# Kernel optimization log

Measured on AMD Instinct MI355X. Metric: run time of the kernel, lower is better.

## Reference

```python
import jax, jax.numpy as jnp
import numpy as np

B, S, D, H, DFF = 2, 4096, 256, 8, 1024
DK = D // H


def setup_inputs() -> dict:
    key = jax.random.key(0)
    ks = jax.random.split(key, 12)
    sc = 0.02
    inp = {
        "x": jax.random.normal(ks[0], (B, S, D), jnp.float32),
        "mask": jnp.ones((B, 1, 1, S), jnp.int32),
        "Wq": jax.random.normal(ks[1], (D, D), jnp.float32) * sc,
        "bq": jnp.zeros((D,), jnp.float32),
        "Wk": jax.random.normal(ks[2], (D, D), jnp.float32) * sc,
        "bk": jnp.zeros((D,), jnp.float32),
        "Wv": jax.random.normal(ks[3], (D, D), jnp.float32) * sc,
        "bv": jnp.zeros((D,), jnp.float32),
        "Wo": jax.random.normal(ks[4], (D, D), jnp.float32) * sc,
        "bo": jnp.zeros((D,), jnp.float32),
        "W1": jax.random.normal(ks[5], (D, DFF), jnp.float32) * sc,
        "b1": jnp.zeros((DFF,), jnp.float32),
        "W2": jax.random.normal(ks[6], (DFF, D), jnp.float32) * sc,
        "b2": jnp.zeros((D,), jnp.float32),
        "g1": jnp.ones((D,), jnp.float32),
        "be1": jnp.zeros((D,), jnp.float32),
        "g2": jnp.ones((D,), jnp.float32),
        "be2": jnp.zeros((D,), jnp.float32),
        "a1": jnp.float32(1e-8),
        "a2": jnp.float32(1e-8),
    }
    return inp


def _layernorm(x, g, b, eps=1e-5):
    mu = jnp.mean(x, axis=-1, keepdims=True)
    var = jnp.var(x, axis=-1, keepdims=True)
    return (x - mu) * jax.lax.rsqrt(var + eps) * g + b


def _block(x, mask, Wq, bq, Wk, bk, Wv, bv, Wo, bo, W1, b1, W2, b2, g1, be1, g2, be2, a1, a2):
    # multi-head attention (dropout = identity in eval)
    def proj(W, b):
        return (x @ W + b).reshape(B, S, H, DK).transpose(0, 2, 1, 3)  # [B,H,S,DK]
    q, k, v = proj(Wq, bq), proj(Wk, bk), proj(Wv, bv)
    scores = jnp.einsum("bhsd,bhtd->bhst", q, k) / jnp.sqrt(jnp.float32(DK))
    scores = jnp.where(mask == 0, jnp.float32(-1e9), scores)
    p_attn = jax.nn.softmax(scores, axis=-1)
    ctx = jnp.einsum("bhst,bhtd->bhsd", p_attn, v)
    ctx = ctx.transpose(0, 2, 1, 3).reshape(B, S, D)
    attn_out = ctx @ Wo + bo
    x1 = _layernorm(x + a1 * attn_out, g1, be1)
    # FFN
    h = jax.nn.gelu(x1 @ W1 + b1, approximate=False)
    ffn_out = h @ W2 + b2
    return _layernorm(x1 + a2 * ffn_out, g2, be2)


def reference(x, mask, Wq, bq, Wk, bk, Wv, bv, Wo, bo, W1, b1, W2, b2, g1, be1, g2, be2, a1, a2):
    return _block(x, mask, Wq, bq, Wk, bk, Wv, bv, Wo, bo, W1, b1, W2, b2, g1, be1, g2, be2, a1, a2)
```

## Files before the change

### kernel.cpp

```cpp
#include <hip/hip_runtime.h>
#include <hip/hip_bf16.h>
#include <math.h>

#define B_ 2
#define S_ 4096
#define D_ 256
#define H_ 8
#define DFF_ 1024
#define DK_ 32

typedef __attribute__((ext_vector_type(8))) short short8;
typedef __attribute__((ext_vector_type(4))) float f32x4;
typedef __attribute__((ext_vector_type(16))) float f32x16;
typedef __attribute__((ext_vector_type(4))) int int4v;

__device__ __forceinline__ unsigned short f2bf(float f) {
  unsigned int u = __builtin_bit_cast(unsigned int, f);
  u += 0x7FFFu + ((u >> 16) & 1u);
  return (unsigned short)(u >> 16);
}

__device__ __forceinline__ float bf2f(unsigned short s) {
  unsigned int u = ((unsigned int)s) << 16;
  return __builtin_bit_cast(float, u);
}

__device__ __forceinline__ short8 u32x4_to_s8(unsigned int a, unsigned int b,
                                              unsigned int c, unsigned int d) {
  int4v v = {(int)a, (int)b, (int)c, (int)d};
  return __builtin_bit_cast(short8, v);
}

__device__ __forceinline__ float gelu_fast(float v) {
  float e = __builtin_amdgcn_exp2f(v * fmaf(0.10294609f, v * v, 2.3022077f));
  float th = 1.0f - 2.0f * __builtin_amdgcn_rcpf(e + 1.0f);
  return 0.5f * v * (1.0f + th);
}

__global__ __launch_bounds__(256) void k_prepw(
    const float* __restrict__ Wq, const float* __restrict__ Wk,
    const float* __restrict__ Wv, const float* __restrict__ Wo,
    const float* __restrict__ W1, const float* __restrict__ W2,
    const float* __restrict__ bq, const float* __restrict__ bk,
    const float* __restrict__ bv, const float* __restrict__ x,
    unsigned short* __restrict__ WqkvT, unsigned short* __restrict__ WoT,
    unsigned short* __restrict__ W1pk, unsigned short* __restrict__ W2pk,
    float* __restrict__ bqkv, unsigned short* __restrict__ xb) {
  const float k2 = 0.25500525551f;
  int bx = blockIdx.x, t = threadIdx.x;

  if (bx < 192) {
    __shared__ float tile[64][65];
    const float* src;
    int Nsz, ti, tj;
    float scale = 1.0f;
    if (bx < 48) {
      int which = bx >> 4, s = bx & 15;
      src = (which == 0) ? Wq : (which == 1) ? Wk : Wv;
      Nsz = 256; ti = s >> 2; tj = s & 3;
      if (which == 0) scale = k2;
    } else if (bx < 64) {
      int s = bx - 48;
      src = Wo; Nsz = 256; ti = s >> 2; tj = s & 3;
    } else if (bx < 128) {
      int s = bx - 64;
      src = W1; Nsz = 1024; ti = s >> 4; tj = s & 15;
    } else {
      int s = bx - 128;
      src = W2; Nsz = 256; ti = s >> 2; tj = s & 3;
    }
    int row0 = ti * 64, col0 = tj * 64;
    int c = t & 63, rg = t >> 6;
#pragma unroll
    for (int i = 0; i < 16; i++) {
      int rr = rg * 16 + i;
      tile[rr][c] = src[(size_t)(row0 + rr) * Nsz + col0 + c] * scale;
    }
    __syncthreads();

    if (bx < 64) {
      unsigned short* dst;
      if (bx < 48) dst = WqkvT + (bx >> 4) * 65536;
      else dst = WoT;
      int k = t & 63;
#pragma unroll
      for (int i = 0; i < 16; i++) {
        int nn = rg * 16 + i;
        dst[(size_t)(col0 + nn) * 256 + row0 + k] = f2bf(tile[k][nn]);
      }
    } else {
      unsigned short* pk = (bx < 128) ? W1pk : W2pk;
      int kst_tot = (bx < 128) ? 8 : 32;
      int lane2 = t & 63, sub2 = t >> 6;
#pragma unroll
      for (int i = 0; i < 2; i++) {
        int subc = sub2 * 2 + i;
        int ntl = subc >> 1, kst = subc & 1;
        short8 o;
#pragma unroll
        for (int e = 0; e < 8; e++)
          o[e] = (short)f2bf(tile[kst * 32 + (lane2 >> 4) * 8 + e][ntl * 16 + (lane2 & 15)]);
        int ntg = tj * 4 + ntl;
        int ksg = ti * 2 + kst;
        *(short8*)(pk + ((size_t)(ntg * kst_tot + ksg) * 64 + lane2) * 8) = o;
      }
    }
  } else if (bx == 192) {
#pragma unroll
    for (int j = 0; j < 3; j++) {
      int i = j * 256 + t;
      if (i < 768)
        bqkv[i] = (i < 256) ? bq[i] * k2 : (i < 512) ? bk[i - 256] : bv[i - 512];
    }
  } else {
    int i = (bx - 193) * 2048 + t * 8;
    f32x4 f0 = *(const f32x4*)(x + i);
    f32x4 f1 = *(const f32x4*)(x + i + 4);
    short8 o;
#pragma unroll
    for (int e = 0; e < 4; e++) { o[e] = (short)f2bf(f0[e]); o[e + 4] = (short)f2bf(f1[e]); }
    *(short8*)(xb + i) = o;
  }
}

__global__ __launch_bounds__(256) void k_gemmqkv(const unsigned short* __restrict__ A,
                                                 const unsigned short* __restrict__ Bt,
                                                 const float* __restrict__ bias,
                                                 unsigned short* __restrict__ qb,
                                                 unsigned short* __restrict__ kpk,
                                                 unsigned short* __restrict__ vpk) {
  const int K = 256;
  __shared__ unsigned short Al[128][40];
  __shared__ unsigned short Bl[128][40];
  const int tid = threadIdx.x;
  const int wid = tid >> 6, lane = tid & 63;
  const int lhi = lane >> 4, llo = lane & 15;
  const int wr = wid >> 1, wc = wid & 1;
  const int rowbase = wr * 64, colbase = wc * 64;
  const int bm = blockIdx.x, bn = blockIdx.y;

  f32x4 zero = {0.f, 0.f, 0.f, 0.f};
  f32x4 acc[4][4];
#pragma unroll
  for (int m = 0; m < 4; m++)
#pragma unroll
    for (int n = 0; n < 4; n++) acc[m][n] = zero;

  const int r0 = tid >> 2, c8 = (tid & 3) * 8;
  const unsigned short* A16a = A + (size_t)(bm * 128 + r0) * K + c8;
  const unsigned short* A16b = A + (size_t)(bm * 128 + r0 + 64) * K + c8;
  const unsigned short* Brow0 = Bt + (size_t)(bn * 128 + r0) * K + c8;
  const unsigned short* Brow1 = Bt + (size_t)(bn * 128 + r0 + 64) * K + c8;

  for (int kb = 0; kb < K; kb += 32) {
    __syncthreads();
    *(short8*)&Al[r0][c8] = *(const short8*)(A16a + kb);
    *(short8*)&Al[r0 + 64][c8] = *(const short8*)(A16b + kb);
    *(short8*)&Bl[r0][c8] = *(const short8*)(Brow0 + kb);
    *(short8*)&Bl[r0 + 64][c8] = *(const short8*)(Brow1 + kb);
    __syncthreads();
    short8 af[4], bf[4];
#pragma unroll
    for (int m = 0; m < 4; m++) af[m] = *(const short8*)&Al[rowbase + m * 16 + llo][lhi * 8];
#pragma unroll
    for (int n = 0; n < 4; n++) bf[n] = *(const short8*)&Bl[colbase + n * 16 + llo][lhi * 8];
#pragma unroll
    for (int m = 0; m < 4; m++)
#pragma unroll
      for (int n = 0; n < 4; n++)
        acc[m][n] = __builtin_amdgcn_mfma_f32_16x16x32_bf16(af[m], bf[n], acc[m][n], 0, 0, 0);
  }

#pragma unroll
  for (int m = 0; m < 4; m++)
#pragma unroll
    for (int n = 0; n < 4; n++)
#pragma unroll
      for (int r = 0; r < 4; r++) {
        int row = bm * 128 + rowbase + m * 16 + lhi * 4 + r;
        int gcol = bn * 128 + colbase + n * 16 + llo;
        int which = gcol >> 8;
        int col0 = gcol & 255;
        float v = acc[m][n][r] + bias[gcol];
        unsigned short bv = f2bf(v);
        int t = row & (S_ - 1), b = row >> 12;
        int h = col0 >> 5;
        if (which == 0) {
          qb[(size_t)row * 256 + col0] = bv;
        } else if (which == 1) {
          int c5 = col0 & 31, jj = (c5 >> 4) & 1, hik = (c5 >> 3) & 1, e = c5 & 7;
          int tile = t >> 6, i = (t >> 5) & 1, l31k = t & 31;
          size_t addr = (((size_t)(b * 8 + h) * 64 + tile) * 4 + i * 2 + jj) * 512 +
                        (hik * 32 + l31k) * 8 + e;
          kpk[addr] = bv;
        } else {
          int d = col0 & 31;
          int x5 = t >> 6, j = (t >> 3) & 7, kk = t & 7;
          size_t addr = (((size_t)(b * 8 + h) * 64 + x5) * 4 + (j >> 1)) * 512 +
                        ((j & 1) * 32 + d) * 8 + kk;
          vpk[addr] = bv;
        }
      }
}

__global__ __launch_bounds__(512) void k_ffn(const unsigned short* __restrict__ x1b,
                                             const unsigned short* __restrict__ W1pk,
                                             const float* __restrict__ b1,
                                             const unsigned short* __restrict__ W2pk,
                                             const float* __restrict__ b2,
                                             const float* __restrict__ alpha,
                                             const float* __restrict__ g,
                                             const float* __restrict__ be,
                                             float* __restrict__ out) {
  __shared__ unsigned short Ax[32][268];
  __shared__ unsigned short Hl[32][268];
  __shared__ float psum[32][8], psq[32][8];
  const int tid = threadIdx.x;
  const int w = tid >> 6, lane = tid & 63;
  const int lhi = lane >> 4, llo = lane & 15;
  const int row0 = blockIdx.x * 32;

  {
    int r = tid >> 4, c0 = (tid & 15) * 16;
    const unsigned short* src = x1b + (size_t)(row0 + r) * 256 + c0;
    *(short8*)&Ax[r][c0] = *(const short8*)(src);
    *(short8*)&Ax[r][c0 + 8] = *(const short8*)(src + 8);
  }
  __syncthreads();

  f32x4 zero4 = {0.f, 0.f, 0.f, 0.f};
  f32x4 acc2[2][2];
#pragma unroll
  for (int m = 0; m < 2; m++)
#pragma unroll
    for (int n = 0; n < 2; n++) acc2[m][n] = zero4;

  for (int c = 0; c < 4; ++c) {
    f32x4 acc1[2][2];
#pragma unroll
    for (int m = 0; m < 2; m++)
#pragma unroll
      for (int n = 0; n < 2; n++) acc1[m][n] = zero4;
    const unsigned short* w1base = W1pk + (size_t)(c * 16 + w * 2) * 4096 + lane * 8;
#pragma unroll
    for (int kb = 0; kb < 8; ++kb) {
      short8 af0 = *(const short8*)&Ax[llo][kb * 32 + lhi * 8];
      short8 af1 = *(const short8*)&Ax[16 + llo][kb * 32 + lhi * 8];
      short8 bf0 = *(const short8*)(w1base + kb * 512);
      short8 bf1 = *(const short8*)(w1base + 4096 + kb * 512);
      acc1[0][0] = __builtin_amdgcn_mfma_f32_16x16x32_bf16(af0, bf0, acc1[0][0], 0, 0, 0);
      acc1[0][1] = __builtin_amdgcn_mfma_f32_16x16x32_bf16(af0, bf1, acc1[0][1], 0, 0, 0);
      acc1[1][0] = __builtin_amdgcn_mfma_f32_16x16x32_bf16(af1, bf0, acc1[1][0], 0, 0, 0);
      acc1[1][1] = __builtin_amdgcn_mfma_f32_16x16x32_bf16(af1, bf1, acc1[1][1], 0, 0, 0);
    }
    __syncthreads();
#pragma unroll
    for (int m = 0; m < 2; m++)
#pragma unroll
      for (int n = 0; n < 2; n++)
#pragma unroll
        for (int r = 0; r < 4; r++) {
          int col = w * 32 + n * 16 + llo;
          float v = acc1[m][n][r] + b1[c * 256 + col];
          Hl[m * 16 + lhi * 4 + r][col] = f2bf(gelu_fast(v));
        }
    __syncthreads();
    const unsigned short* w2base = W2pk + (size_t)(w * 2) * 16384 + (size_t)(c * 8) * 512 + lane * 8;
#pragma unroll
    for (int kk = 0; kk < 8; ++kk) {
      short8 a0 = *(const short8*)&Hl[llo][kk * 32 + lhi * 8];
      short8 a1 = *(const short8*)&Hl[16 + llo][kk * 32 + lhi * 8];
      short8 bf0 = *(const short8*)(w2base + kk * 512);
      short8 bf1 = *(const short8*)(w2base + 16384 + kk * 512);
      acc2[0][0] = __builtin_amdgcn_mfma_f32_16x16x32_bf16(a0, bf0, acc2[0][0], 0, 0, 0);
      acc2[0][1] = __builtin_amdgcn_mfma_f32_16x16x32_bf16(a0, bf1, acc2[0][1], 0, 0, 0);
      acc2[1][0] = __builtin_amdgcn_mfma_f32_16x16x32_bf16(a1, bf0, acc2[1][0], 0, 0, 0);
      acc2[1][1] = __builtin_amdgcn_mfma_f32_16x16x32_bf16(a1, bf1, acc2[1][1], 0, 0, 0);
    }
  }

  const float a = alpha[0];
#pragma unroll
  for (int m = 0; m < 2; m++)
#pragma unroll
    for (int r = 0; r < 4; r++) {
      int lrow = m * 16 + lhi * 4 + r;
      float s = 0.f, q = 0.f;
#pragma unroll
      for (int n = 0; n < 2; n++) {
        int col = w * 32 + n * 16 + llo;
        float v = acc2[m][n][r] + b2[col];
        float xv = bf2f(Ax[lrow][col]);
        float rr = fmaf(a, v, xv);
        acc2[m][n][r] = rr;
        s += rr;
        q = fmaf(rr, rr, q);
      }
#pragma unroll
      for (int off = 1; off < 16; off <<= 1) {
        s += __shfl_xor(s, off);
        q += __shfl_xor(q, off);
      }
      if (llo == 0) { psum[lrow][w] = s; psq[lrow][w] = q; }
    }
  __syncthreads();
#pragma unroll
  for (int m = 0; m < 2; m++)
#pragma unroll
    for (int r = 0; r < 4; r++) {
      int lrow = m * 16 + lhi * 4 + r;
      size_t grow = (size_t)(row0 + lrow);
      float S = 0.f, Q = 0.f;
#pragma unroll
      for (int j = 0; j < 8; j++) { S += psum[lrow][j]; Q += psq[lrow][j]; }
      float mu = S * (1.0f / 256.0f);
      float var = Q * (1.0f / 256.0f) - mu * mu;
      float rs = rsqrtf(var + 1e-5f);
#pragma unroll
      for (int n = 0; n < 2; n++) {
        int col = w * 32 + n * 16 + llo;
        out[grow * 256 + col] = (acc2[m][n][r] - mu) * rs * g[col] + be[col];
      }
    }
}

template <int BASE16, int OUT32>
__global__ __launch_bounds__(512) void k_gemmln(const unsigned short* __restrict__ A,
                                                const unsigned short* __restrict__ Bt,
                                                const float* __restrict__ bias,
                                                const void* __restrict__ base,
                                                const float* __restrict__ alpha,
                                                const float* __restrict__ g,
                                                const float* __restrict__ be,
                                                void* __restrict__ y, int K) {
  __shared__ unsigned short Al[2][32][40];
  __shared__ unsigned short Bl[2][256][40];
  __shared__ float psum[32][4], psq[32][4];
  float* partial = (float*)&Bl[0][0][0];

  const int tid = threadIdx.x;
  const int w = tid >> 6, lane = tid & 63;
  const int kh = w >> 2, wc = w & 3;
  const int lhi = lane >> 4, llo = lane & 15;
  const int row0 = blockIdx.x * 32;
  const int Kh = K >> 1;

  f32x4 zero = {0.f, 0.f, 0.f, 0.f};
  f32x4 acc[2][4];
#pragma unroll
  for (int m = 0; m < 2; m++)
#pragma unroll
    for (int n = 0; n < 4; n++) acc[m][n] = zero;

  for (int kb = 0; kb < Kh; kb += 32) {
    __syncthreads();
    if (tid < 256) {
      int kh2 = tid >> 7, ra = (tid >> 2) & 31, ca = (tid & 3) * 8;
      *(short8*)&Al[kh2][ra][ca] =
          *(const short8*)(A + (size_t)(row0 + ra) * K + kh2 * Kh + kb + ca);
    }
#pragma unroll
    for (int s = 0; s < 4; s++) {
      int c = tid + s * 512;
      int kh2 = c >> 10, rb = (c >> 2) & 255, cb = (c & 3) * 8;
      *(short8*)&Bl[kh2][rb][cb] =
          *(const short8*)(Bt + (size_t)rb * K + kh2 * Kh + kb + cb);
    }
    __syncthreads();
    short8 af[2], bf[4];
#pragma unroll
    for (int m = 0; m < 2; m++) af[m] = *(const short8*)&Al[kh][m * 16 + llo][lhi * 8];
#pragma unroll
    for (int n = 0; n < 4; n++)
      bf[n] = *(const short8*)&Bl[kh][wc * 64 + n * 16 + llo][lhi * 8];
#pragma unroll
    for (int m = 0; m < 2; m++)
#pragma unroll
      for (int n = 0; n < 4; n++)
        acc[m][n] = __builtin_amdgcn_mfma_f32_16x16x32_bf16(af[m], bf[n], acc[m][n], 0, 0, 0);
  }

  __syncthreads();
  if (kh == 1) {
#pragma unroll
    for (int m = 0; m < 2; m++)
#pragma unroll
      for (int n = 0; n < 4; n++)
#pragma unroll
        for (int r = 0; r < 4; r++) {
          int lrow = m * 16 + lhi * 4 + r;
          int col = wc * 64 + n * 16 + llo;
          partial[lrow * 256 + col] = acc[m][n][r];
        }
  }
  __syncthreads();

  const float a = alpha[0];
  const unsigned short* b16 = (const unsigned short*)base;
  const float* b32 = (const float*)base;

  if (kh == 0) {
#pragma unroll
    for (int m = 0; m < 2; m++)
#pragma unroll
      for (int r = 0; r < 4; r++) {
        int lrow = m * 16 + lhi * 4 + r;
        size_t grow = (size_t)(row0 + lrow);
        float s = 0.f, q = 0.f;
#pragma unroll
        for (int n = 0; n < 4; n++) {
          int col = wc * 64 + n * 16 + llo;
          float v = acc[m][n][r] + partial[lrow * 256 + col] + bias[col];
          float xb = BASE16 ? bf2f(b16[grow * 256 + col]) : b32[grow * 256 + col];
          float rr = fmaf(a, v, xb);
          acc[m][n][r] = rr;
          s += rr;
          q = fmaf(rr, rr, q);
        }
#pragma unroll
        for (int off = 1; off < 16; off <<= 1) {
          s += __shfl_xor(s, off);
          q += __shfl_xor(q, off);
        }
        if (llo == 0) { psum[lrow][wc] = s; psq[lrow][wc] = q; }
      }
  }
  __syncthreads();

  if (kh == 0) {
#pragma unroll
    for (int m = 0; m < 2; m++)
#pragma unroll
      for (int r = 0; r < 4; r++) {
        int lrow = m * 16 + lhi * 4 + r;
        size_t grow = (size_t)(row0 + lrow);
        float S = psum[lrow][0] + psum[lrow][1] + psum[lrow][2] + psum[lrow][3];
        float Q = psq[lrow][0] + psq[lrow][1] + psq[lrow][2] + psq[lrow][3];
        float mu = S * (1.0f / 256.0f);
        float var = Q * (1.0f / 256.0f) - mu * mu;
        float rs = rsqrtf(var + 1e-5f);
#pragma unroll
        for (int n = 0; n < 4; n++) {
          int col = wc * 64 + n * 16 + llo;
          float o = (acc[m][n][r] - mu) * rs * g[col] + be[col];
          if (OUT32) ((float*)y)[grow * 256 + col] = o;
          else ((unsigned short*)y)[grow * 256 + col] = f2bf(o);
        }
      }
  }
}

__global__ __launch_bounds__(256, 2) void k_attn(const unsigned short* __restrict__ qbuf,
                                                 const unsigned short* __restrict__ kpk,
                                                 const unsigned short* __restrict__ vpk,
                                                 const int* __restrict__ mask,
                                                 unsigned short* __restrict__ ctx) {
  __shared__ float accS[4][64][32];
  __shared__ float lS[4][64];
  const int tid = threadIdx.x;
  const int lane = tid & 63;
  const int w = tid >> 6;
  const int l31 = lane & 31, hi = lane >> 5;
  const int q0 = blockIdx.x * 64;
  const int h = blockIdx.y, b = blockIdx.z;
  const size_t bS = (size_t)b * S_;

  const unsigned short* QpA = qbuf + (bS + q0 + l31) * 256 + h * DK_ + hi * 8;
  short8 qa0 = *(const short8*)QpA;
  short8 qa1 = *(const short8*)(QpA + 16);
  const unsigned short* QpB = QpA + 32 * 256;
  short8 qb0 = *(const short8*)QpB;
  short8 qb1 = *(const short8*)(QpB + 16);

  const size_t fragbase = ((size_t)(b * H_ + h) * 64 + w * 16) * 2048 + lane * 8;
  const unsigned short* kp = kpk + fragbase;
  const unsigned short* vp = vpk + fragbase;
  const int* mp = mask + bS + w * 1024 + lane;

  f32x16 accA, accB, laccA, laccB;
#pragma unroll
  for (int r = 0; r < 16; r++) { accA[r] = 0.f; accB[r] = 0.f; laccA[r] = 0.f; laccB[r] = 0.f; }
  const f32x16 zz = accA;
  short8 ones;
#pragma unroll
  for (int e = 0; e < 8; e++) ones[e] = (short)0x3F80;

  short8 kA[4], vA[4], kB[4], vB[4];
  unsigned int pk0[8], pk1[8];
  f32x16 s0, s1;
  int tcur = 0;
  int mvC, mvN;

#define LDK(DST) { DST[0] = *(const short8*)(kp); DST[1] = *(const short8*)(kp + 512); \
                   DST[2] = *(const short8*)(kp + 1024); DST[3] = *(const short8*)(kp + 1536); kp += 2048; }
#define LDV(DST) { DST[0] = *(const short8*)(vp); DST[1] = *(const short8*)(vp + 512); \
                   DST[2] = *(const short8*)(vp + 1024); DST[3] = *(const short8*)(vp + 1536); vp += 2048; }
#define QKM(KF, qx0, qx1) {                                                      \
    s0 = __builtin_amdgcn_mfma_f32_32x32x16_bf16(KF[0], qx0, zz, 0, 0, 0);       \
    s1 = __builtin_amdgcn_mfma_f32_32x32x16_bf16(KF[2], qx0, zz, 0, 0, 0);       \
    s0 = __builtin_amdgcn_mfma_f32_32x32x16_bf16(KF[1], qx1, s0, 0, 0, 0);       \
    s1 = __builtin_amdgcn_mfma_f32_32x32x16_bf16(KF[3], qx1, s1, 0, 0, 0);       \
  }
#define EXPM(bal) {                                                              \
    if (__builtin_expect((bal) != ~0ull, 0)) {                                   \
      _Pragma("unroll") for (int r = 0; r < 16; r++) {                           \
        int tt = (r & 3) + 8 * (r >> 2) + 4 * hi;                                \
        if (!(((bal) >> tt) & 1)) s0[r] = -3e38f;                                \
        if (!(((bal) >> (tt + 32)) & 1)) s1[r] = -3e38f;                         \
      }                                                                          \
    }                                                                            \
    _Pragma("unroll") for (int r = 0; r < 16; r++) {                             \
      s0[r] = __builtin_amdgcn_exp2f(s0[r]);                                     \
      s1[r] = __builtin_amdgcn_exp2f(s1[r]);                                     \
    }                                                                            \
    _Pragma("unroll") for (int j = 0; j < 8; j++) {                              \
      asm("v_cvt_pk_bf16_f32 %0, %1, %2" : "=v"(pk0[j]) : "v"(s0[2*j]), "v"(s0[2*j+1])); \
      asm("v_cvt_pk_bf16_f32 %0, %1, %2" : "=v"(pk1[j]) : "v"(s1[2*j]), "v"(s1[2*j+1])); \
    }                                                                            \
  }
#define PVM(VF, accX, laccX) {                                                   \
    __builtin_amdgcn_s_setprio(1);                                               \
    _Pragma("unroll") for (int kk = 0; kk < 4; kk++) {                           \
      unsigned int* pk = (kk < 2) ? pk0 : pk1;                                   \
      int base = (kk & 1) * 4;                                                   \
      auto r02 = __builtin_amdgcn_permlane32_swap(pk[base], pk[base + 2], false, false);     \
      auto r13 = __builtin_amdgcn_permlane32_swap(pk[base + 1], pk[base + 3], false, false); \
      short8 pfr = u32x4_to_s8(r02[0], r13[0], r02[1], r13[1]);                  \
      accX = __builtin_amdgcn_mfma_f32_32x32x16_bf16(pfr, VF[kk], accX, 0, 0, 0);\
      laccX = __builtin_amdgcn_mfma_f32_32x32x16_bf16(pfr, ones, laccX, 0, 0, 0);\
    }                                                                            \
    __builtin_amdgcn_s_setprio(0);                                               \
  }
#define TILESTEP(KC, VC, KN, VN) {                                               \
    unsigned long long bal = __ballot(mvC != 0);                                 \
    QKM(KC, qa0, qa1);                                                           \
    LDK(KN);                                                                     \
    EXPM(bal);                                                                   \
    PVM(VC, accA, laccA);                                                        \
    QKM(KC, qb0, qb1);                                                           \
    LDV(VN);                                                                     \
    EXPM(bal);                                                                   \
    PVM(VC, accB, laccB);                                                        \
    mvC = mvN;                                                                   \
    tcur++;                                                                      \
    mvN = mp[(tcur + 1 < 16 ? tcur + 1 : 15) * 64];                              \
  }

  LDK(kA);
  LDV(vA);
  mvC = mp[0];
  mvN = mp[64];

  for (int it = 0; it < 8; ++it) {
    TILESTEP(kA, vA, kB, vB);
    TILESTEP(kB, vB, kA, vA);
  }

#pragma unroll
  for (int r = 0; r < 16; r++) {
    int q = (r & 3) + 8 * (r >> 2) + 4 * hi;
    accS[w][q][l31] = accA[r];
    accS[w][q + 32][l31] = accB[r];
  }
  if (l31 == 0) {
#pragma unroll
    for (int r = 0; r < 16; r++) {
      int q = (r & 3) + 8 * (r >> 2) + 4 * hi;
      lS[w][q] = laccA[r];
      lS[w][q + 32] = laccB[r];
    }
  }
  __syncthreads();
#pragma unroll
  for (int i = 0; i < 8; i++) {
    int e = tid + 256 * i;
    int q = e >> 5, d = e & 31;
    float o = accS[0][q][d] + accS[1][q][d] + accS[2][q][d] + accS[3][q][d];
    float L = lS[0][q] + lS[1][q] + lS[2][q] + lS[3][q];
    ctx[(bS + q0 + q) * (size_t)D_ + h * DK_ + d] = f2bf(o / L);
  }
#undef LDK
#undef LDV
#undef QKM
#undef EXPM
#undef PVM
#undef TILESTEP
}

extern "C" void kernel_launch(void* const* d_in, const int* in_sizes, int n_in,
                              void* d_out, int out_size, void* d_ws, size_t ws_size,
                              hipStream_t stream) {
  const float* x   = (const float*)d_in[0];
  const int* mask  = (const int*)d_in[1];
  const float* Wq  = (const float*)d_in[2];
  const float* bq  = (const float*)d_in[3];
  const float* Wk  = (const float*)d_in[4];
  const float* bk  = (const float*)d_in[5];
  const float* Wv  = (const float*)d_in[6];
  const float* bv  = (const float*)d_in[7];
  const float* Wo  = (const float*)d_in[8];
  const float* bo  = (const float*)d_in[9];
  const float* W1  = (const float*)d_in[10];
  const float* b1  = (const float*)d_in[11];
  const float* W2  = (const float*)d_in[12];
  const float* b2  = (const float*)d_in[13];
  const float* g1  = (const float*)d_in[14];
  const float* be1 = (const float*)d_in[15];
  const float* g2  = (const float*)d_in[16];
  const float* be2 = (const float*)d_in[17];
  const float* a1  = (const float*)d_in[18];
  const float* a2  = (const float*)d_in[19];
  float* out = (float*)d_out;

  char* ws = (char*)d_ws;
  const size_t MB = 1024 * 1024;
  unsigned short* qb  = (unsigned short*)(ws + 0);
  unsigned short* kpk = (unsigned short*)(ws + 5 * MB);
  unsigned short* vpk = (unsigned short*)(ws + 10 * MB);
  unsigned short* ctx = (unsigned short*)(ws + 15 * MB);
  unsigned short* x1b = (unsigned short*)(ws + 19 * MB);
  unsigned short* WqkvT = (unsigned short*)(ws + 40 * MB);
  unsigned short* WoT   = (unsigned short*)(ws + 40 * MB + 512 * 1024);
  unsigned short* W1pk  = (unsigned short*)(ws + 41 * MB);
  unsigned short* W2pk  = (unsigned short*)(ws + 41 * MB + 512 * 1024);
  float* bqkv           = (float*)(ws + 42 * MB);
  unsigned short* xb    = (unsigned short*)(ws + 43 * MB);

  const int NTOK = B_ * S_;

  k_prepw<<<dim3(1217), 256, 0, stream>>>(Wq, Wk, Wv, Wo, W1, W2, bq, bk, bv, x,
                                          WqkvT, WoT, W1pk, W2pk, bqkv, xb);

  k_gemmqkv<<<dim3(64, 6), 256, 0, stream>>>(xb, WqkvT, bqkv, qb, kpk, vpk);

  k_attn<<<dim3(S_ / 64, H_, B_), 256, 0, stream>>>(qb, kpk, vpk, mask, ctx);

  k_gemmln<0, 0><<<dim3(NTOK / 32), 512, 0, stream>>>(ctx, WoT, bo, x, a1, g1, be1,
                                                      x1b, 256);

  k_ffn<<<dim3(NTOK / 32), 512, 0, stream>>>(x1b, W1pk, b1, W2pk, b2, a2, g2, be2, out);
}
```

Before: 112.5 us.

## Prepack Wo into MFMA fragment layout and halve QKV GEMM row tile

Wo is now written by the prep kernel in the same MFMA-fragment packed layout as W1/W2. A new output-projection kernel loads B fragments straight from global memory without LDS staging. It also drops the split-K partial reduction through shared memory that the old generic GEMM+LayerNorm kernel used. Separately, the QKV GEMM tile drops from 128 to 64 rows, doubling the grid to improve CU occupancy, at the cost of re-reading the weight tile more often.

```diff
diff --git a/kernel.cpp b/kernel.cpp
--- a/kernel.cpp
+++ b/kernel.cpp
@@ -43,7 +43,7 @@
     const float* __restrict__ W1, const float* __restrict__ W2,
     const float* __restrict__ bq, const float* __restrict__ bk,
     const float* __restrict__ bv, const float* __restrict__ x,
-    unsigned short* __restrict__ WqkvT, unsigned short* __restrict__ WoT,
+    unsigned short* __restrict__ WqkvT, unsigned short* __restrict__ Wopk,
     unsigned short* __restrict__ W1pk, unsigned short* __restrict__ W2pk,
     float* __restrict__ bqkv, unsigned short* __restrict__ xb) {
   const float k2 = 0.25500525551f;
@@ -78,10 +78,8 @@
     }
     __syncthreads();
 
-    if (bx < 64) {
-      unsigned short* dst;
-      if (bx < 48) dst = WqkvT + (bx >> 4) * 65536;
-      else dst = WoT;
+    if (bx < 48) {
+      unsigned short* dst = WqkvT + (bx >> 4) * 65536;
       int k = t & 63;
 #pragma unroll
       for (int i = 0; i < 16; i++) {
@@ -89,7 +87,7 @@
         dst[(size_t)(col0 + nn) * 256 + row0 + k] = f2bf(tile[k][nn]);
       }
     } else {
-      unsigned short* pk = (bx < 128) ? W1pk : W2pk;
+      unsigned short* pk = (bx < 64) ? Wopk : (bx < 128) ? W1pk : W2pk;
       int kst_tot = (bx < 128) ? 8 : 32;
       int lane2 = t & 63, sub2 = t >> 6;
 #pragma unroll
@@ -130,54 +128,52 @@
                                                  unsigned short* __restrict__ kpk,
                                                  unsigned short* __restrict__ vpk) {
   const int K = 256;
-  __shared__ unsigned short Al[128][40];
+  __shared__ unsigned short Al[64][40];
   __shared__ unsigned short Bl[128][40];
   const int tid = threadIdx.x;
   const int wid = tid >> 6, lane = tid & 63;
   const int lhi = lane >> 4, llo = lane & 15;
   const int wr = wid >> 1, wc = wid & 1;
-  const int rowbase = wr * 64, colbase = wc * 64;
+  const int rowbase = wr * 32, colbase = wc * 64;
   const int bm = blockIdx.x, bn = blockIdx.y;
 
   f32x4 zero = {0.f, 0.f, 0.f, 0.f};
-  f32x4 acc[4][4];
-#pragma unroll
-  for (int m = 0; m < 4; m++)
+  f32x4 acc[2][4];
+#pragma unroll
+  for (int m = 0; m < 2; m++)
 #pragma unroll
     for (int n = 0; n < 4; n++) acc[m][n] = zero;
 
   const int r0 = tid >> 2, c8 = (tid & 3) * 8;
-  const unsigned short* A16a = A + (size_t)(bm * 128 + r0) * K + c8;
-  const unsigned short* A16b = A + (size_t)(bm * 128 + r0 + 64) * K + c8;
+  const unsigned short* A16 = A + (size_t)(bm * 64 + r0) * K + c8;
   const unsigned short* Brow0 = Bt + (size_t)(bn * 128 + r0) * K + c8;
   const unsigned short* Brow1 = Bt + (size_t)(bn * 128 + r0 + 64) * K + c8;
 
   for (int kb = 0; kb < K; kb += 32) {
     __syncthreads();
-    *(short8*)&Al[r0][c8] = *(const short8*)(A16a + kb);
-    *(short8*)&Al[r0 + 64][c8] = *(const short8*)(A16b + kb);
+    *(short8*)&Al[r0][c8] = *(const short8*)(A16 + kb);
     *(short8*)&Bl[r0][c8] = *(const short8*)(Brow0 + kb);
     *(short8*)&Bl[r0 + 64][c8] = *(const short8*)(Brow1 + kb);
     __syncthreads();
-    short8 af[4], bf[4];
-#pragma unroll
-    for (int m = 0; m < 4; m++) af[m] = *(const short8*)&Al[rowbase + m * 16 + llo][lhi * 8];
+    short8 af[2], bf[4];
+#pragma unroll
+    for (int m = 0; m < 2; m++) af[m] = *(const short8*)&Al[rowbase + m * 16 + llo][lhi * 8];
 #pragma unroll
     for (int n = 0; n < 4; n++) bf[n] = *(const short8*)&Bl[colbase + n * 16 + llo][lhi * 8];
 #pragma unroll
-    for (int m = 0; m < 4; m++)
+    for (int m = 0; m < 2; m++)
 #pragma unroll
       for (int n = 0; n < 4; n++)
         acc[m][n] = __builtin_amdgcn_mfma_f32_16x16x32_bf16(af[m], bf[n], acc[m][n], 0, 0, 0);
   }
 
 #pragma unroll
-  for (int m = 0; m < 4; m++)
+  for (int m = 0; m < 2; m++)
 #pragma unroll
     for (int n = 0; n < 4; n++)
 #pragma unroll
       for (int r = 0; r < 4; r++) {
-        int row = bm * 128 + rowbase + m * 16 + lhi * 4 + r;
+        int row = bm * 64 + rowbase + m * 16 + lhi * 4 + r;
         int gcol = bn * 128 + colbase + n * 16 + llo;
         int which = gcol >> 8;
         int col0 = gcol & 255;
@@ -203,6 +199,95 @@
       }
 }
 
+__global__ __launch_bounds__(512) void k_wo(const unsigned short* __restrict__ ctx,
+                                            const unsigned short* __restrict__ Wopk,
+                                            const float* __restrict__ bo,
+                                            const float* __restrict__ xbase,
+                                            const float* __restrict__ alpha,
+                                            const float* __restrict__ g,
+                                            const float* __restrict__ be,
+                                            unsigned short* __restrict__ x1b) {
+  __shared__ unsigned short Ax[32][268];
+  __shared__ float psum[32][8], psq[32][8];
+  const int tid = threadIdx.x;
+  const int w = tid >> 6, lane = tid & 63;
+  const int lhi = lane >> 4, llo = lane & 15;
+  const int row0 = blockIdx.x * 32;
+
+  {
+    int r = tid >> 4, c0 = (tid & 15) * 16;
+    const unsigned short* src = ctx + (size_t)(row0 + r) * 256 + c0;
+    *(short8*)&Ax[r][c0] = *(const short8*)(src);
+    *(short8*)&Ax[r][c0 + 8] = *(const short8*)(src + 8);
+  }
+  __syncthreads();
+
+  f32x4 zero4 = {0.f, 0.f, 0.f, 0.f};
+  f32x4 acc[2][2];
+#pragma unroll
+  for (int m = 0; m < 2; m++)
+#pragma unroll
+    for (int n = 0; n < 2; n++) acc[m][n] = zero4;
+
+  const unsigned short* wobase = Wopk + (size_t)(w * 2) * 4096 + lane * 8;
+#pragma unroll
+  for (int kb = 0; kb < 8; ++kb) {
+    short8 af0 = *(const short8*)&Ax[llo][kb * 32 + lhi * 8];
+    short8 af1 = *(const short8*)&Ax[16 + llo][kb * 32 + lhi * 8];
+    short8 bf0 = *(const short8*)(wobase + kb * 512);
+    short8 bf1 = *(const short8*)(wobase + 4096 + kb * 512);
+    acc[0][0] = __builtin_amdgcn_mfma_f32_16x16x32_bf16(af0, bf0, acc[0][0], 0, 0, 0);
+    acc[0][1] = __builtin_amdgcn_mfma_f32_16x16x32_bf16(af0, bf1, acc[0][1], 0, 0, 0);
+    acc[1][0] = __builtin_amdgcn_mfma_f32_16x16x32_bf16(af1, bf0, acc[1][0], 0, 0, 0);
+    acc[1][1] = __builtin_amdgcn_mfma_f32_16x16x32_bf16(af1, bf1, acc[1][1], 0, 0, 0);
+  }
+
+  const float a = alpha[0];
+#pragma unroll
+  for (int m = 0; m < 2; m++)
+#pragma unroll
+    for (int r = 0; r < 4; r++) {
+      int lrow = m * 16 + lhi * 4 + r;
+      size_t grow = (size_t)(row0 + lrow);
+      float s = 0.f, q = 0.f;
+#pragma unroll
+      for (int n = 0; n < 2; n++) {
+        int col = w * 32 + n * 16 + llo;
+        float v = acc[m][n][r] + bo[col];
+        float xv = xbase[grow * 256 + col];
+        float rr = fmaf(a, v, xv);
+        acc[m][n][r] = rr;
+        s += rr;
+        q = fmaf(rr, rr, q);
+      }
+#pragma unroll
+      for (int off = 1; off < 16; off <<= 1) {
+        s += __shfl_xor(s, off);
+        q += __shfl_xor(q, off);
+      }
+      if (llo == 0) { psum[lrow][w] = s; psq[lrow][w] = q; }
+    }
+  __syncthreads();
+#pragma unroll
+  for (int m = 0; m < 2; m++)
+#pragma unroll
+    for (int r = 0; r < 4; r++) {
+      int lrow = m * 16 + lhi * 4 + r;
+      size_t grow = (size_t)(row0 + lrow);
+      float S = 0.f, Q = 0.f;
+#pragma unroll
+      for (int j = 0; j < 8; j++) { S += psum[lrow][j]; Q += psq[lrow][j]; }
+      float mu = S * (1.0f / 256.0f);
+      float var = Q * (1.0f / 256.0f) - mu * mu;
+      float rs = rsqrtf(var + 1e-5f);
+#pragma unroll
+      for (int n = 0; n < 2; n++) {
+        int col = w * 32 + n * 16 + llo;
+        x1b[grow * 256 + col] = f2bf((acc[m][n][r] - mu) * rs * g[col] + be[col]);
+      }
+    }
+}
+
 __global__ __launch_bounds__(512) void k_ffn(const unsigned short* __restrict__ x1b,
                                              const unsigned short* __restrict__ W1pk,
                                              const float* __restrict__ b1,
@@ -322,132 +407,6 @@
         out[grow * 256 + col] = (acc2[m][n][r] - mu) * rs * g[col] + be[col];
       }
     }
-}
-
-template <int BASE16, int OUT32>
-__global__ __launch_bounds__(512) void k_gemmln(const unsigned short* __restrict__ A,
-                                                const unsigned short* __restrict__ Bt,
-                                                const float* __restrict__ bias,
-                                                const void* __restrict__ base,
-                                                const float* __restrict__ alpha,
-                                                const float* __restrict__ g,
-                                                const float* __restrict__ be,
-                                                void* __restrict__ y, int K) {
-  __shared__ unsigned short Al[2][32][40];
-  __shared__ unsigned short Bl[2][256][40];
-  __shared__ float psum[32][4], psq[32][4];
-  float* partial = (float*)&Bl[0][0][0];
-
-  const int tid = threadIdx.x;
-  const int w = tid >> 6, lane = tid & 63;
-  const int kh = w >> 2, wc = w & 3;
-  const int lhi = lane >> 4, llo = lane & 15;
-  const int row0 = blockIdx.x * 32;
-  const int Kh = K >> 1;
-
-  f32x4 zero = {0.f, 0.f, 0.f, 0.f};
-  f32x4 acc[2][4];
-#pragma unroll
-  for (int m = 0; m < 2; m++)
-#pragma unroll
-    for (int n = 0; n < 4; n++) acc[m][n] = zero;
-
-  for (int kb = 0; kb < Kh; kb += 32) {
-    __syncthreads();
-    if (tid < 256) {
-      int kh2 = tid >> 7, ra = (tid >> 2) & 31, ca = (tid & 3) * 8;
-      *(short8*)&Al[kh2][ra][ca] =
-          *(const short8*)(A + (size_t)(row0 + ra) * K + kh2 * Kh + kb + ca);
-    }
-#pragma unroll
-    for (int s = 0; s < 4; s++) {
-      int c = tid + s * 512;
-      int kh2 = c >> 10, rb = (c >> 2) & 255, cb = (c & 3) * 8;
-      *(short8*)&Bl[kh2][rb][cb] =
-          *(const short8*)(Bt + (size_t)rb * K + kh2 * Kh + kb + cb);
-    }
-    __syncthreads();
-    short8 af[2], bf[4];
-#pragma unroll
-    for (int m = 0; m < 2; m++) af[m] = *(const short8*)&Al[kh][m * 16 + llo][lhi * 8];
-#pragma unroll
-    for (int n = 0; n < 4; n++)
-      bf[n] = *(const short8*)&Bl[kh][wc * 64 + n * 16 + llo][lhi * 8];
-#pragma unroll
-    for (int m = 0; m < 2; m++)
-#pragma unroll
-      for (int n = 0; n < 4; n++)
-        acc[m][n] = __builtin_amdgcn_mfma_f32_16x16x32_bf16(af[m], bf[n], acc[m][n], 0, 0, 0);
-  }
-
-  __syncthreads();
-  if (kh == 1) {
-#pragma unroll
-    for (int m = 0; m < 2; m++)
-#pragma unroll
-      for (int n = 0; n < 4; n++)
-#pragma unroll
-        for (int r = 0; r < 4; r++) {
-          int lrow = m * 16 + lhi * 4 + r;
-          int col = wc * 64 + n * 16 + llo;
-          partial[lrow * 256 + col] = acc[m][n][r];
-        }
-  }
-  __syncthreads();
-
-  const float a = alpha[0];
-  const unsigned short* b16 = (const unsigned short*)base;
-  const float* b32 = (const float*)base;
-
-  if (kh == 0) {
-#pragma unroll
-    for (int m = 0; m < 2; m++)
-#pragma unroll
-      for (int r = 0; r < 4; r++) {
-        int lrow = m * 16 + lhi * 4 + r;
-        size_t grow = (size_t)(row0 + lrow);
-        float s = 0.f, q = 0.f;
-#pragma unroll
-        for (int n = 0; n < 4; n++) {
-          int col = wc * 64 + n * 16 + llo;
-          float v = acc[m][n][r] + partial[lrow * 256 + col] + bias[col];
-          float xb = BASE16 ? bf2f(b16[grow * 256 + col]) : b32[grow * 256 + col];
-          float rr = fmaf(a, v, xb);
-          acc[m][n][r] = rr;
-          s += rr;
-          q = fmaf(rr, rr, q);
-        }
-#pragma unroll
-        for (int off = 1; off < 16; off <<= 1) {
-          s += __shfl_xor(s, off);
-          q += __shfl_xor(q, off);
-        }
-        if (llo == 0) { psum[lrow][wc] = s; psq[lrow][wc] = q; }
-      }
-  }
-  __syncthreads();
-
-  if (kh == 0) {
-#pragma unroll
-    for (int m = 0; m < 2; m++)
-#pragma unroll
-      for (int r = 0; r < 4; r++) {
-        int lrow = m * 16 + lhi * 4 + r;
-        size_t grow = (size_t)(row0 + lrow);
-        float S = psum[lrow][0] + psum[lrow][1] + psum[lrow][2] + psum[lrow][3];
-        float Q = psq[lrow][0] + psq[lrow][1] + psq[lrow][2] + psq[lrow][3];
-        float mu = S * (1.0f / 256.0f);
-        float var = Q * (1.0f / 256.0f) - mu * mu;
-        float rs = rsqrtf(var + 1e-5f);
-#pragma unroll
-        for (int n = 0; n < 4; n++) {
-          int col = wc * 64 + n * 16 + llo;
-          float o = (acc[m][n][r] - mu) * rs * g[col] + be[col];
-          if (OUT32) ((float*)y)[grow * 256 + col] = o;
-          else ((unsigned short*)y)[grow * 256 + col] = f2bf(o);
-        }
-      }
-  }
 }
 
 __global__ __launch_bounds__(256, 2) void k_attn(const unsigned short* __restrict__ qbuf,
@@ -620,7 +579,7 @@
   unsigned short* ctx = (unsigned short*)(ws + 15 * MB);
   unsigned short* x1b = (unsigned short*)(ws + 19 * MB);
   unsigned short* WqkvT = (unsigned short*)(ws + 40 * MB);
-  unsigned short* WoT   = (unsigned short*)(ws + 40 * MB + 512 * 1024);
+  unsigned short* Wopk  = (unsigned short*)(ws + 40 * MB + 512 * 1024);
   unsigned short* W1pk  = (unsigned short*)(ws + 41 * MB);
   unsigned short* W2pk  = (unsigned short*)(ws + 41 * MB + 512 * 1024);
   float* bqkv           = (float*)(ws + 42 * MB);
@@ -629,14 +588,13 @@
   const int NTOK = B_ * S_;
 
   k_prepw<<<dim3(1217), 256, 0, stream>>>(Wq, Wk, Wv, Wo, W1, W2, bq, bk, bv, x,
-                                          WqkvT, WoT, W1pk, W2pk, bqkv, xb);
-
-  k_gemmqkv<<<dim3(64, 6), 256, 0, stream>>>(xb, WqkvT, bqkv, qb, kpk, vpk);
+                                          WqkvT, Wopk, W1pk, W2pk, bqkv, xb);
+
+  k_gemmqkv<<<dim3(128, 6), 256, 0, stream>>>(xb, WqkvT, bqkv, qb, kpk, vpk);
 
   k_attn<<<dim3(S_ / 64, H_, B_), 256, 0, stream>>>(qb, kpk, vpk, mask, ctx);
 
-  k_gemmln<0, 0><<<dim3(NTOK / 32), 512, 0, stream>>>(ctx, WoT, bo, x, a1, g1, be1,
-                                                      x1b, 256);
+  k_wo<<<dim3(NTOK / 32), 512, 0, stream>>>(ctx, Wopk, bo, x, a1, g1, be1, x1b);
 
   k_ffn<<<dim3(NTOK / 32), 512, 0, stream>>>(x1b, W1pk, b1, W2pk, b2, a2, g2, be2, out);
 }
```

New measurement: 108.6 us. 1.04x faster.
